# Performance work log

Measured on AMD Instinct MI355X. Metric: run time of the kernel, lower is better.

## Reference

```python
import jax, jax.numpy as jnp
import numpy as np

D_MODEL = 1024
NUM_HEADS = 16
DEPTH = D_MODEL // NUM_HEADS


def setup_inputs() -> dict:
    key = jax.random.key(0)
    ks = jax.random.split(key, 6)
    B, S = 2, 2048
    scale = 1.0 / np.sqrt(D_MODEL)
    return {
        "q": jax.random.normal(ks[0], (B, S, D_MODEL), jnp.float32),
        "k": jax.random.normal(ks[1], (B, S, D_MODEL), jnp.float32),
        "v": jax.random.normal(ks[2], (B, S, D_MODEL), jnp.float32),
        "wq": jax.random.normal(ks[3], (D_MODEL, D_MODEL), jnp.float32) * scale,
        "wk": jax.random.normal(ks[4], (D_MODEL, D_MODEL), jnp.float32) * scale,
        "wv": jax.random.normal(ks[5], (D_MODEL, D_MODEL), jnp.float32) * scale,
    }


def reference(q, k, v, wq, wk, wv):
    B, S, _ = q.shape
    # Linear projections (nn.Linear: x @ W.T), then split heads -> [B,H,S,depth]
    def split(x):
        return x.reshape(B, -1, NUM_HEADS, DEPTH).transpose(0, 2, 1, 3)
    Q = split(q @ wq.T)
    K = split(k @ wk.T)
    V = split(v @ wv.T)
    scores = jnp.einsum("bhqd,bhkd->bhqk", Q, K) / np.sqrt(DEPTH).astype(np.float32)
    attn = jax.nn.softmax(scores, axis=-1)
    out = jnp.einsum("bhqk,bhkd->bhqd", attn, V)
    # merge heads; note: original forward never applies self.dense
    return out.transpose(0, 2, 1, 3).reshape(B, S, D_MODEL)
```

## Files before the change

kernel.cpp:

```cpp
#include <hip/hip_runtime.h>
#include <hip/hip_bf16.h>
#include <stdint.h>

#define B_SZ 2
#define S_LEN 2048
#define DM 1024
#define NH 16
#define DEPTH 64
#define M_ROWS (B_SZ * S_LEN)
#define SCALE_Q 0.1803368801111144f

typedef __attribute__((ext_vector_type(8))) short bf16x8;
typedef __attribute__((ext_vector_type(4))) float f32x4;

__device__ __forceinline__ unsigned short f2bf(float x) {
    union { float f; unsigned u; } a; a.f = x;
    unsigned r = a.u + 0x7FFF + ((a.u >> 16) & 1);
    return (unsigned short)(r >> 16);
}

__device__ __forceinline__ void async_ld16(const unsigned short* g, unsigned short* l) {
    __builtin_amdgcn_global_load_lds(
        (const __attribute__((address_space(1))) void*)g,
        (__attribute__((address_space(3))) void*)l,
        16, 0, 0);
}


__global__ __launch_bounds__(256)
void convert_kernel(const float* __restrict__ q, const float* __restrict__ k,
                    const float* __restrict__ v, const float* __restrict__ wq,
                    const float* __restrict__ wk, const float* __restrict__ wv,
                    unsigned short* __restrict__ dst) {
    const int z = blockIdx.y;
    const float* src = (z == 0) ? q : (z == 1) ? k : (z == 2) ? v
                     : (z == 3) ? wq : (z == 4) ? wk : wv;
    const size_t n4  = (z < 3) ? ((size_t)M_ROWS * DM / 4) : ((size_t)DM * DM / 4);
    const size_t off = (z < 3) ? ((size_t)z * M_ROWS * DM)
                               : ((size_t)3 * M_ROWS * DM + (size_t)(z - 3) * DM * DM);
    unsigned short* d = dst + off;
    const size_t stride = (size_t)gridDim.x * blockDim.x;
    for (size_t i = (size_t)blockIdx.x * blockDim.x + threadIdx.x; i < n4; i += stride) {
        float4 x = ((const float4*)src)[i];
        ushort4 p;
        p.x = f2bf(x.x); p.y = f2bf(x.y); p.z = f2bf(x.z); p.w = f2bf(x.w);
        ((ushort4*)d)[i] = p;
    }
}

__global__ __launch_bounds__(256)
void proj_gemm2_kernel(const unsigned short* __restrict__ Xall,
                       const unsigned short* __restrict__ Wall,
                       unsigned short* __restrict__ Call) {
    __shared__ unsigned short As[128 * 64];
    __shared__ unsigned short Bs[128 * 64];

    const int z = blockIdx.z;
    const unsigned short* X = Xall + (size_t)z * M_ROWS * DM;
    const unsigned short* W = Wall + (size_t)z * DM * DM;
    unsigned short* C = Call + (size_t)z * M_ROWS * DM;

    const int tid  = threadIdx.x;
    const int wave = tid >> 6;
    const int lane = tid & 63;
    const int quad = lane >> 4;
    const int l16  = lane & 15;
    const int m0 = blockIdx.x * 128;
    const int n0 = blockIdx.y * 128;
    const int wm = (wave >> 1) * 64;
    const int wn = (wave & 1) * 64;

    const int sr = lane >> 3;
    const int sc = (lane & 7) ^ sr;

    f32x4 acc[4][4];
#pragma unroll
    for (int mt = 0; mt < 4; ++mt)
#pragma unroll
        for (int nt = 0; nt < 4; ++nt)
            acc[mt][nt] = (f32x4){0.f, 0.f, 0.f, 0.f};

    for (int k0 = 0; k0 < DM; k0 += 64) {
#pragma unroll
        for (int i = 0; i < 4; ++i) {
            const int r = i * 32 + wave * 8 + sr;
            async_ld16(X + (size_t)(m0 + r) * DM + k0 + sc * 8,
                       (unsigned short*)((char*)As + i * 4096 + wave * 1024));
            async_ld16(W + (size_t)(n0 + r) * DM + k0 + sc * 8,
                       (unsigned short*)((char*)Bs + i * 4096 + wave * 1024));
        }
        __syncthreads();

#pragma unroll
        for (int kc = 0; kc < 2; ++kc) {
            bf16x8 af[4], bfr[4];
#pragma unroll
            for (int mt = 0; mt < 4; ++mt) {
                const int row = wm + mt * 16 + l16;
                af[mt] = *(const bf16x8*)&As[row * 64 + (((kc * 4 + quad) ^ (row & 7)) * 8)];
            }
#pragma unroll
            for (int nt = 0; nt < 4; ++nt) {
                const int row = wn + nt * 16 + l16;
                bfr[nt] = *(const bf16x8*)&Bs[row * 64 + (((kc * 4 + quad) ^ (row & 7)) * 8)];
            }
#pragma unroll
            for (int mt = 0; mt < 4; ++mt)
#pragma unroll
                for (int nt = 0; nt < 4; ++nt)
                    acc[mt][nt] = __builtin_amdgcn_mfma_f32_16x16x32_bf16(
                        af[mt], bfr[nt], acc[mt][nt], 0, 0, 0);
        }
        __syncthreads();
    }

    const float scale = (z == 0) ? SCALE_Q : 1.0f;
#pragma unroll
    for (int mt = 0; mt < 4; ++mt)
#pragma unroll
        for (int nt = 0; nt < 4; ++nt)
#pragma unroll
            for (int r = 0; r < 4; ++r) {
                const int row = m0 + wm + mt * 16 + quad * 4 + r;
                const int col = n0 + wn + nt * 16 + l16;
                C[(size_t)row * DM + col] = f2bf(acc[mt][nt][r] * scale);
            }
}

__global__ __launch_bounds__(256)
void vtrans_kernel(const unsigned short* __restrict__ Vp,
                   unsigned short* __restrict__ Vt) {
    __shared__ unsigned short Ls[64 * 72];
    const int tr = blockIdx.x;
    const int h  = blockIdx.y;
    const int tid = threadIdx.x;

#pragma unroll
    for (int i = 0; i < 2; ++i) {
        const int id = i * 256 + tid;
        const int r = id >> 3, c = id & 7;
        bf16x8 v8 = *(const bf16x8*)&Vp[(size_t)(tr * 64 + r) * DM + h * 64 + c * 8];
        *(bf16x8*)&Ls[r * 72 + ((c ^ (r & 7)) * 8)] = v8;
    }
    __syncthreads();

    const int b = tr >> 5;
    const int col0 = (tr & 31) * 64;
#pragma unroll
    for (int i = 0; i < 2; ++i) {
        const int id = i * 256 + tid;
        const int d = id >> 3, c2 = id & 7;
        unsigned short tmp[8];
#pragma unroll
        for (int j = 0; j < 8; ++j) {
            const int t = c2 * 8 + j;
            tmp[j] = Ls[t * 72 + (((d >> 3) ^ (t & 7)) * 8) + (d & 7)];
        }
        *(bf16x8*)&Vt[(size_t)((b * NH + h) * DEPTH + d) * S_LEN + col0 + c2 * 8] =
            *(const bf16x8*)tmp;
    }
}

__global__ __launch_bounds__(256)
void attn2_kernel(const unsigned short* __restrict__ Qp,
                  const unsigned short* __restrict__ Kp,
                  const unsigned short* __restrict__ Vt,
                  float* __restrict__ out) {
    __shared__ unsigned short Ks[64 * 64];
    __shared__ unsigned short Vs[64 * 64];
    __shared__ unsigned short Ps[4 * 16 * 72];

    const int tid  = threadIdx.x;
    const int wave = tid >> 6;
    const int lane = tid & 63;
    const int quad = lane >> 4;
    const int l16  = lane & 15;
    const int q0 = blockIdx.x * 64;
    const int h  = blockIdx.y;
    const int b  = blockIdx.z;

    const int sr = lane >> 3;
    const int sc = (lane & 7) ^ sr;

    const unsigned short* Kg = Kp + (size_t)(b * S_LEN) * DM + h * DEPTH;
    const unsigned short* Vg = Vt + (size_t)((b * NH + h) * DEPTH) * S_LEN;

    bf16x8 qf[2];
    {
        const unsigned short* p =
            Qp + (size_t)(b * S_LEN + q0 + wave * 16 + l16) * DM + h * DEPTH;
        qf[0] = *(const bf16x8*)(p + quad * 8);
        qf[1] = *(const bf16x8*)(p + 32 + quad * 8);
    }

    f32x4 accO[4];
    float lacc[4];
#pragma unroll
    for (int f = 0; f < 4; ++f) accO[f] = (f32x4){0.f, 0.f, 0.f, 0.f};
#pragma unroll
    for (int r = 0; r < 4; ++r) lacc[r] = 0.f;

    unsigned short* PsW = &Ps[wave * 16 * 72];

    for (int t0 = 0; t0 < S_LEN; t0 += 64) {
#pragma unroll
        for (int i = 0; i < 2; ++i) {
            const int r = i * 32 + wave * 8 + sr;
            async_ld16(Kg + (size_t)(t0 + r) * DM + sc * 8,
                       (unsigned short*)((char*)Ks + i * 4096 + wave * 1024));
            async_ld16(Vg + (size_t)r * S_LEN + t0 + sc * 8,
                       (unsigned short*)((char*)Vs + i * 4096 + wave * 1024));
        }
        __syncthreads();

        f32x4 sc4[4];
#pragma unroll
        for (int nt = 0; nt < 4; ++nt) {
            const int row = nt * 16 + l16;
            bf16x8 kf0 = *(const bf16x8*)&Ks[row * 64 + ((quad ^ (row & 7)) * 8)];
            bf16x8 kf1 = *(const bf16x8*)&Ks[row * 64 + (((4 + quad) ^ (row & 7)) * 8)];
            f32x4 a = (f32x4){0.f, 0.f, 0.f, 0.f};
            a = __builtin_amdgcn_mfma_f32_16x16x32_bf16(qf[0], kf0, a, 0, 0, 0);
            a = __builtin_amdgcn_mfma_f32_16x16x32_bf16(qf[1], kf1, a, 0, 0, 0);
            sc4[nt] = a;
        }

#pragma unroll
        for (int nt = 0; nt < 4; ++nt)
#pragma unroll
            for (int r = 0; r < 4; ++r) {
                float p = __builtin_amdgcn_exp2f(sc4[nt][r]);
                union { float f; unsigned u; } cv; cv.f = p;
                union { unsigned u; float f; } tv; tv.u = cv.u & 0xFFFF0000u;
                lacc[r] += tv.f;
                PsW[(quad * 4 + r) * 72 + nt * 16 + l16] = (unsigned short)(cv.u >> 16);
            }

        bf16x8 pf0 = *(const bf16x8*)&PsW[l16 * 72 + quad * 8];
        bf16x8 pf1 = *(const bf16x8*)&PsW[l16 * 72 + 32 + quad * 8];

#pragma unroll
        for (int f = 0; f < 4; ++f) {
            const int row = f * 16 + l16;
            bf16x8 vf0 = *(const bf16x8*)&Vs[row * 64 + ((quad ^ (row & 7)) * 8)];
            bf16x8 vf1 = *(const bf16x8*)&Vs[row * 64 + (((4 + quad) ^ (row & 7)) * 8)];
            accO[f] = __builtin_amdgcn_mfma_f32_16x16x32_bf16(pf0, vf0, accO[f], 0, 0, 0);
            accO[f] = __builtin_amdgcn_mfma_f32_16x16x32_bf16(pf1, vf1, accO[f], 0, 0, 0);
        }
        __syncthreads();
    }

#pragma unroll
    for (int r = 0; r < 4; ++r)
#pragma unroll
        for (int off = 1; off < 16; off <<= 1)
            lacc[r] += __shfl_xor(lacc[r], off, 64);

#pragma unroll
    for (int f = 0; f < 4; ++f)
#pragma unroll
        for (int r = 0; r < 4; ++r) {
            const size_t row = (size_t)(b * S_LEN + q0 + wave * 16 + quad * 4 + r);
            out[row * DM + h * DEPTH + f * 16 + l16] = accO[f][r] / lacc[r];
        }
}

#define LDK 72

__global__ __launch_bounds__(256)
void proj_gemm_kernel(const float* __restrict__ q, const float* __restrict__ k,
                      const float* __restrict__ v, const float* __restrict__ wq,
                      const float* __restrict__ wk, const float* __restrict__ wv,
                      unsigned short* __restrict__ Qp, unsigned short* __restrict__ Kp,
                      unsigned short* __restrict__ Vp) {
    __shared__ unsigned short As[128 * LDK];
    __shared__ unsigned short Bs[128 * LDK];

    const int z = blockIdx.z;
    const float* __restrict__ X = (z == 0) ? q : (z == 1) ? k : v;
    const float* __restrict__ W = (z == 0) ? wq : (z == 1) ? wk : wv;
    unsigned short* __restrict__ C = (z == 0) ? Qp : (z == 1) ? Kp : Vp;

    const int tid  = threadIdx.x;
    const int wave = tid >> 6;
    const int lane = tid & 63;
    const int quad = lane >> 4;
    const int l16  = lane & 15;
    const int m0 = blockIdx.x * 128;
    const int n0 = blockIdx.y * 128;
    const int wm = (wave >> 1) * 64;
    const int wn = (wave & 1) * 64;

    f32x4 acc[4][4];
#pragma unroll
    for (int mt = 0; mt < 4; ++mt)
#pragma unroll
        for (int nt = 0; nt < 4; ++nt)
            acc[mt][nt] = (f32x4){0.f, 0.f, 0.f, 0.f};

    for (int k0 = 0; k0 < DM; k0 += 64) {
#pragma unroll
        for (int vv = 0; vv < 8; ++vv) {
            int vecid = tid + 256 * vv;
            int r  = vecid >> 4;
            int c4 = vecid & 15;
            const float4 xa = *(const float4*)&X[(size_t)(m0 + r) * DM + k0 + c4 * 4];
            ushort4 pa;
            pa.x = f2bf(xa.x); pa.y = f2bf(xa.y); pa.z = f2bf(xa.z); pa.w = f2bf(xa.w);
            *(ushort4*)&As[r * LDK + c4 * 4] = pa;
            const float4 xb = *(const float4*)&W[(size_t)(n0 + r) * DM + k0 + c4 * 4];
            ushort4 pb;
            pb.x = f2bf(xb.x); pb.y = f2bf(xb.y); pb.z = f2bf(xb.z); pb.w = f2bf(xb.w);
            *(ushort4*)&Bs[r * LDK + c4 * 4] = pb;
        }
        __syncthreads();

#pragma unroll
        for (int kc = 0; kc < 2; ++kc) {
            bf16x8 af[4], bfr[4];
#pragma unroll
            for (int mt = 0; mt < 4; ++mt)
                af[mt] = *(const bf16x8*)&As[(wm + mt * 16 + l16) * LDK + kc * 32 + quad * 8];
#pragma unroll
            for (int nt = 0; nt < 4; ++nt)
                bfr[nt] = *(const bf16x8*)&Bs[(wn + nt * 16 + l16) * LDK + kc * 32 + quad * 8];
#pragma unroll
            for (int mt = 0; mt < 4; ++mt)
#pragma unroll
                for (int nt = 0; nt < 4; ++nt)
                    acc[mt][nt] = __builtin_amdgcn_mfma_f32_16x16x32_bf16(
                        af[mt], bfr[nt], acc[mt][nt], 0, 0, 0);
        }
        __syncthreads();
    }

#pragma unroll
    for (int mt = 0; mt < 4; ++mt)
#pragma unroll
        for (int nt = 0; nt < 4; ++nt)
#pragma unroll
            for (int r = 0; r < 4; ++r) {
                int row = m0 + wm + mt * 16 + quad * 4 + r;
                int col = n0 + wn + nt * 16 + l16;
                C[(size_t)row * DM + col] = f2bf(acc[mt][nt][r]);
            }
}

__global__ __launch_bounds__(256)
void attn_kernel(const unsigned short* __restrict__ Qp,
                 const unsigned short* __restrict__ Kp,
                 const unsigned short* __restrict__ Vp,
                 float* __restrict__ out) {
    __shared__ unsigned short Ks[64 * LDK];
    __shared__ unsigned short Vtl[64 * LDK];
    __shared__ unsigned short Ps[4 * 16 * LDK];

    const int tid  = threadIdx.x;
    const int wave = tid >> 6;
    const int lane = tid & 63;
    const int quad = lane >> 4;
    const int l16  = lane & 15;
    const int q0 = blockIdx.x * 64;
    const int h  = blockIdx.y;
    const int b  = blockIdx.z;
    const int wbase = wave * 16 * LDK;

    bf16x8 qf[2];
    {
        size_t row = (size_t)b * S_LEN + q0 + wave * 16 + l16;
        const unsigned short* p = Qp + row * DM + h * DEPTH;
        qf[0] = *(const bf16x8*)(p + quad * 8);
        qf[1] = *(const bf16x8*)(p + 32 + quad * 8);
    }

    float m_i[4], l_i[4];
    f32x4 accO[4];
#pragma unroll
    for (int r = 0; r < 4; ++r) { m_i[r] = -1e30f; l_i[r] = 0.f; }
#pragma unroll
    for (int f = 0; f < 4; ++f) accO[f] = (f32x4){0.f, 0.f, 0.f, 0.f};

    for (int t0 = 0; t0 < S_LEN; t0 += 64) {
#pragma unroll
        for (int vv = 0; vv < 2; ++vv) {
            int vecid = tid + 256 * vv;
            int r  = vecid >> 3;
            int cv = vecid & 7;
            size_t grow = (size_t)(b * S_LEN + t0 + r) * DM + h * DEPTH + cv * 8;
            *(bf16x8*)&Ks[r * LDK + cv * 8] = *(const bf16x8*)(Kp + grow);
            bf16x8 vvv = *(const bf16x8*)(Vp + grow);
#pragma unroll
            for (int j = 0; j < 8; ++j)
                Vtl[(cv * 8 + j) * LDK + r] = ((const unsigned short*)&vvv)[j];
        }
        __syncthreads();

        f32x4 sc4[4];
#pragma unroll
        for (int nt = 0; nt < 4; ++nt) {
            f32x4 a = (f32x4){0.f, 0.f, 0.f, 0.f};
            bf16x8 kf0 = *(const bf16x8*)&Ks[(nt * 16 + l16) * LDK + quad * 8];
            bf16x8 kf1 = *(const bf16x8*)&Ks[(nt * 16 + l16) * LDK + 32 + quad * 8];
            a = __builtin_amdgcn_mfma_f32_16x16x32_bf16(qf[0], kf0, a, 0, 0, 0);
            a = __builtin_amdgcn_mfma_f32_16x16x32_bf16(qf[1], kf1, a, 0, 0, 0);
            sc4[nt] = a;
        }
#pragma unroll
        for (int nt = 0; nt < 4; ++nt)
#pragma unroll
            for (int r = 0; r < 4; ++r) sc4[nt][r] *= 0.125f;

#pragma unroll
        for (int r = 0; r < 4; ++r) {
            float mx = fmaxf(fmaxf(sc4[0][r], sc4[1][r]), fmaxf(sc4[2][r], sc4[3][r]));
#pragma unroll
            for (int off = 1; off < 16; off <<= 1)
                mx = fmaxf(mx, __shfl_xor(mx, off, 64));
            float mnew = fmaxf(m_i[r], mx);
            float alpha = __expf(m_i[r] - mnew);
            float rs = 0.f;
#pragma unroll
            for (int nt = 0; nt < 4; ++nt) {
                float p = __expf(sc4[nt][r] - mnew);
                sc4[nt][r] = p;
                rs += p;
            }
#pragma unroll
            for (int off = 1; off < 16; off <<= 1)
                rs += __shfl_xor(rs, off, 64);
            l_i[r] = l_i[r] * alpha + rs;
            m_i[r] = mnew;
#pragma unroll
            for (int f = 0; f < 4; ++f) accO[f][r] *= alpha;
        }

#pragma unroll
        for (int nt = 0; nt < 4; ++nt)
#pragma unroll
            for (int r = 0; r < 4; ++r)
                Ps[wbase + (quad * 4 + r) * LDK + nt * 16 + l16] = f2bf(sc4[nt][r]);
        __syncthreads();

        bf16x8 pf0 = *(const bf16x8*)&Ps[wbase + l16 * LDK + quad * 8];
        bf16x8 pf1 = *(const bf16x8*)&Ps[wbase + l16 * LDK + 32 + quad * 8];
#pragma unroll
        for (int f = 0; f < 4; ++f) {
            bf16x8 vf0 = *(const bf16x8*)&Vtl[(f * 16 + l16) * LDK + quad * 8];
            bf16x8 vf1 = *(const bf16x8*)&Vtl[(f * 16 + l16) * LDK + 32 + quad * 8];
            accO[f] = __builtin_amdgcn_mfma_f32_16x16x32_bf16(pf0, vf0, accO[f], 0, 0, 0);
            accO[f] = __builtin_amdgcn_mfma_f32_16x16x32_bf16(pf1, vf1, accO[f], 0, 0, 0);
        }
        __syncthreads();
    }

#pragma unroll
    for (int f = 0; f < 4; ++f)
#pragma unroll
        for (int r = 0; r < 4; ++r) {
            size_t row = (size_t)b * S_LEN + q0 + wave * 16 + quad * 4 + r;
            out[row * DM + h * DEPTH + f * 16 + l16] = accO[f][r] / l_i[r];
        }
}

extern "C" void kernel_launch(void* const* d_in, const int* in_sizes, int n_in,
                              void* d_out, int out_size, void* d_ws, size_t ws_size,
                              hipStream_t stream) {
    const float* q  = (const float*)d_in[0];
    const float* k  = (const float*)d_in[1];
    const float* v  = (const float*)d_in[2];
    const float* wq = (const float*)d_in[3];
    const float* wk = (const float*)d_in[4];
    const float* wv = (const float*)d_in[5];
    float* out = (float*)d_out;

    unsigned short* ws = (unsigned short*)d_ws;
    const size_t NPROJ = (size_t)M_ROWS * DM;
    const size_t NW    = (size_t)DM * DM;

    const size_t need = (3 * NPROJ + 3 * NW + 3 * NPROJ) * sizeof(unsigned short);

    if (ws_size >= need) {
        unsigned short* Xbf = ws;
        unsigned short* Wbf = ws + 3 * NPROJ;
        unsigned short* Cp  = ws + 3 * NPROJ + 3 * NW;
        unsigned short* Qp  = Cp;
        unsigned short* Kp  = Cp + NPROJ;
        unsigned short* Vp  = Cp + 2 * NPROJ;
        unsigned short* Vt  = ws;

        convert_kernel<<<dim3(256, 6), 256, 0, stream>>>(q, k, v, wq, wk, wv, Xbf);
        proj_gemm2_kernel<<<dim3(M_ROWS / 128, DM / 128, 3), 256, 0, stream>>>(Xbf, Wbf, Cp);
        vtrans_kernel<<<dim3(M_ROWS / 64, NH), 256, 0, stream>>>(Vp, Vt);
        attn2_kernel<<<dim3(S_LEN / 64, NH, B_SZ), 256, 0, stream>>>(Qp, Kp, Vt, out);
    } else {
        unsigned short* Qp = ws;
        unsigned short* Kp = ws + NPROJ;
        unsigned short* Vp = ws + 2 * NPROJ;
        proj_gemm_kernel<<<dim3(M_ROWS / 128, DM / 128, 3), 256, 0, stream>>>(
            q, k, v, wq, wk, wv, Qp, Kp, Vp);
        attn_kernel<<<dim3(S_LEN / 64, NH, B_SZ), 256, 0, stream>>>(Qp, Kp, Vp, out);
    }
}
```

Before: 214.2 us.

## Switch projection GEMM and attention to 32x32x16 MFMA with larger query tiles

Both the projection GEMM and the attention kernel move from 16x16x32 to 32x32x16 bf16 MFMA tiles. Attention blocks now cover 128 queries (32 per wave), which halves K/V reloads per query. The V transpose permutes key order so the packed P stores line up with the new layout. The aim is fewer fragment LDS reads per flop and higher MFMA throughput, at the cost of more accumulator registers and possibly lower occupancy, with only half as many attention blocks.

```diff
diff --git a/kernel.cpp b/kernel.cpp
--- a/kernel.cpp
+++ b/kernel.cpp
@@ -12,6 +12,7 @@
 
 typedef __attribute__((ext_vector_type(8))) short bf16x8;
 typedef __attribute__((ext_vector_type(4))) float f32x4;
+typedef __attribute__((ext_vector_type(16))) float f32x16;
 
 __device__ __forceinline__ unsigned short f2bf(float x) {
     union { float f; unsigned u; } a; a.f = x;
@@ -19,7 +20,7 @@
     return (unsigned short)(r >> 16);
 }
 
-__device__ __forceinline__ void async_ld16(const unsigned short* g, unsigned short* l) {
+__device__ __forceinline__ void async_ld16(const unsigned short* g, void* l) {
     __builtin_amdgcn_global_load_lds(
         (const __attribute__((address_space(1))) void*)g,
         (__attribute__((address_space(3))) void*)l,
@@ -49,7 +50,7 @@
 }
 
 __global__ __launch_bounds__(256)
-void proj_gemm2_kernel(const unsigned short* __restrict__ Xall,
+void proj_gemm3_kernel(const unsigned short* __restrict__ Xall,
                        const unsigned short* __restrict__ Wall,
                        unsigned short* __restrict__ Call) {
     __shared__ unsigned short As[128 * 64];
@@ -63,67 +64,68 @@
     const int tid  = threadIdx.x;
     const int wave = tid >> 6;
     const int lane = tid & 63;
-    const int quad = lane >> 4;
-    const int l16  = lane & 15;
+    const int l32  = lane & 31;
+    const int s    = lane >> 5;
     const int m0 = blockIdx.x * 128;
     const int n0 = blockIdx.y * 128;
     const int wm = (wave >> 1) * 64;
     const int wn = (wave & 1) * 64;
 
-    const int sr = lane >> 3;
-    const int sc = (lane & 7) ^ sr;
-
-    f32x4 acc[4][4];
-#pragma unroll
-    for (int mt = 0; mt < 4; ++mt)
-#pragma unroll
-        for (int nt = 0; nt < 4; ++nt)
-            acc[mt][nt] = (f32x4){0.f, 0.f, 0.f, 0.f};
+    const int r8 = lane >> 3;
+    const int sc = (lane & 7) ^ r8;
+
+    f32x16 acc[2][2];
+#pragma unroll
+    for (int mi = 0; mi < 2; ++mi)
+#pragma unroll
+        for (int ni = 0; ni < 2; ++ni)
+#pragma unroll
+            for (int r = 0; r < 16; ++r) acc[mi][ni][r] = 0.f;
 
     for (int k0 = 0; k0 < DM; k0 += 64) {
 #pragma unroll
         for (int i = 0; i < 4; ++i) {
-            const int r = i * 32 + wave * 8 + sr;
+            const int r = i * 32 + wave * 8 + r8;
             async_ld16(X + (size_t)(m0 + r) * DM + k0 + sc * 8,
-                       (unsigned short*)((char*)As + i * 4096 + wave * 1024));
+                       (char*)As + i * 4096 + wave * 1024);
             async_ld16(W + (size_t)(n0 + r) * DM + k0 + sc * 8,
-                       (unsigned short*)((char*)Bs + i * 4096 + wave * 1024));
-        }
-        __syncthreads();
-
-#pragma unroll
-        for (int kc = 0; kc < 2; ++kc) {
-            bf16x8 af[4], bfr[4];
-#pragma unroll
-            for (int mt = 0; mt < 4; ++mt) {
-                const int row = wm + mt * 16 + l16;
-                af[mt] = *(const bf16x8*)&As[row * 64 + (((kc * 4 + quad) ^ (row & 7)) * 8)];
-            }
-#pragma unroll
-            for (int nt = 0; nt < 4; ++nt) {
-                const int row = wn + nt * 16 + l16;
-                bfr[nt] = *(const bf16x8*)&Bs[row * 64 + (((kc * 4 + quad) ^ (row & 7)) * 8)];
-            }
-#pragma unroll
-            for (int mt = 0; mt < 4; ++mt)
-#pragma unroll
-                for (int nt = 0; nt < 4; ++nt)
-                    acc[mt][nt] = __builtin_amdgcn_mfma_f32_16x16x32_bf16(
-                        af[mt], bfr[nt], acc[mt][nt], 0, 0, 0);
+                       (char*)Bs + i * 4096 + wave * 1024);
+        }
+        __syncthreads();
+
+#pragma unroll
+        for (int ch = 0; ch < 4; ++ch) {
+            bf16x8 af[2], bfr[2];
+#pragma unroll
+            for (int mi = 0; mi < 2; ++mi) {
+                const int row = wm + mi * 32 + l32;
+                af[mi] = *(const bf16x8*)&As[row * 64 + (((2 * ch + s) ^ (row & 7)) * 8)];
+            }
+#pragma unroll
+            for (int ni = 0; ni < 2; ++ni) {
+                const int row = wn + ni * 32 + l32;
+                bfr[ni] = *(const bf16x8*)&Bs[row * 64 + (((2 * ch + s) ^ (row & 7)) * 8)];
+            }
+#pragma unroll
+            for (int mi = 0; mi < 2; ++mi)
+#pragma unroll
+                for (int ni = 0; ni < 2; ++ni)
+                    acc[mi][ni] = __builtin_amdgcn_mfma_f32_32x32x16_bf16(
+                        af[mi], bfr[ni], acc[mi][ni], 0, 0, 0);
         }
         __syncthreads();
     }
 
     const float scale = (z == 0) ? SCALE_Q : 1.0f;
 #pragma unroll
-    for (int mt = 0; mt < 4; ++mt)
-#pragma unroll
-        for (int nt = 0; nt < 4; ++nt)
-#pragma unroll
-            for (int r = 0; r < 4; ++r) {
-                const int row = m0 + wm + mt * 16 + quad * 4 + r;
-                const int col = n0 + wn + nt * 16 + l16;
-                C[(size_t)row * DM + col] = f2bf(acc[mt][nt][r] * scale);
+    for (int mi = 0; mi < 2; ++mi)
+#pragma unroll
+        for (int ni = 0; ni < 2; ++ni)
+#pragma unroll
+            for (int r = 0; r < 16; ++r) {
+                const int row = m0 + wm + mi * 32 + (r & 3) + 8 * (r >> 2) + 4 * s;
+                const int col = n0 + wn + ni * 32 + l32;
+                C[(size_t)row * DM + col] = f2bf(acc[mi][ni][r] * scale);
             }
 }
 
@@ -153,7 +155,8 @@
         unsigned short tmp[8];
 #pragma unroll
         for (int j = 0; j < 8; ++j) {
-            const int t = c2 * 8 + j;
+            const int cc = c2 * 8 + j;
+            const int t = (cc >> 1) + ((cc & 1) << 5);
             tmp[j] = Ls[t * 72 + (((d >> 3) ^ (t & 7)) * 8) + (d & 7)];
         }
         *(bf16x8*)&Vt[(size_t)((b * NH + h) * DEPTH + d) * S_LEN + col0 + c2 * 8] =
@@ -162,106 +165,121 @@
 }
 
 __global__ __launch_bounds__(256)
-void attn2_kernel(const unsigned short* __restrict__ Qp,
+void attn3_kernel(const unsigned short* __restrict__ Qp,
                   const unsigned short* __restrict__ Kp,
                   const unsigned short* __restrict__ Vt,
                   float* __restrict__ out) {
     __shared__ unsigned short Ks[64 * 64];
     __shared__ unsigned short Vs[64 * 64];
-    __shared__ unsigned short Ps[4 * 16 * 72];
+    __shared__ unsigned short Ps[4 * 32 * 72];
 
     const int tid  = threadIdx.x;
     const int wave = tid >> 6;
     const int lane = tid & 63;
-    const int quad = lane >> 4;
-    const int l16  = lane & 15;
-    const int q0 = blockIdx.x * 64;
+    const int l32  = lane & 31;
+    const int s    = lane >> 5;
+    const int q0 = blockIdx.x * 128;
     const int h  = blockIdx.y;
     const int b  = blockIdx.z;
 
-    const int sr = lane >> 3;
-    const int sc = (lane & 7) ^ sr;
+    const int r8 = lane >> 3;
+    const int sc = (lane & 7) ^ r8;
 
     const unsigned short* Kg = Kp + (size_t)(b * S_LEN) * DM + h * DEPTH;
     const unsigned short* Vg = Vt + (size_t)((b * NH + h) * DEPTH) * S_LEN;
 
-    bf16x8 qf[2];
+    bf16x8 qf[4];
     {
         const unsigned short* p =
-            Qp + (size_t)(b * S_LEN + q0 + wave * 16 + l16) * DM + h * DEPTH;
-        qf[0] = *(const bf16x8*)(p + quad * 8);
-        qf[1] = *(const bf16x8*)(p + 32 + quad * 8);
-    }
-
-    f32x4 accO[4];
-    float lacc[4];
-#pragma unroll
-    for (int f = 0; f < 4; ++f) accO[f] = (f32x4){0.f, 0.f, 0.f, 0.f};
-#pragma unroll
-    for (int r = 0; r < 4; ++r) lacc[r] = 0.f;
-
-    unsigned short* PsW = &Ps[wave * 16 * 72];
+            Qp + (size_t)(b * S_LEN + q0 + wave * 32 + l32) * DM + h * DEPTH;
+#pragma unroll
+        for (int ch = 0; ch < 4; ++ch)
+            qf[ch] = *(const bf16x8*)(p + ch * 16 + s * 8);
+    }
+
+    f32x16 oacc[2];
+    float lacc[16];
+#pragma unroll
+    for (int d = 0; d < 2; ++d)
+#pragma unroll
+        for (int r = 0; r < 16; ++r) oacc[d][r] = 0.f;
+#pragma unroll
+    for (int r = 0; r < 16; ++r) lacc[r] = 0.f;
+
+    unsigned short* PsW = &Ps[wave * 32 * 72];
 
     for (int t0 = 0; t0 < S_LEN; t0 += 64) {
 #pragma unroll
         for (int i = 0; i < 2; ++i) {
-            const int r = i * 32 + wave * 8 + sr;
+            const int r = i * 32 + wave * 8 + r8;
             async_ld16(Kg + (size_t)(t0 + r) * DM + sc * 8,
-                       (unsigned short*)((char*)Ks + i * 4096 + wave * 1024));
+                       (char*)Ks + i * 4096 + wave * 1024);
             async_ld16(Vg + (size_t)r * S_LEN + t0 + sc * 8,
-                       (unsigned short*)((char*)Vs + i * 4096 + wave * 1024));
-        }
-        __syncthreads();
-
-        f32x4 sc4[4];
-#pragma unroll
-        for (int nt = 0; nt < 4; ++nt) {
-            const int row = nt * 16 + l16;
-            bf16x8 kf0 = *(const bf16x8*)&Ks[row * 64 + ((quad ^ (row & 7)) * 8)];
-            bf16x8 kf1 = *(const bf16x8*)&Ks[row * 64 + (((4 + quad) ^ (row & 7)) * 8)];
-            f32x4 a = (f32x4){0.f, 0.f, 0.f, 0.f};
-            a = __builtin_amdgcn_mfma_f32_16x16x32_bf16(qf[0], kf0, a, 0, 0, 0);
-            a = __builtin_amdgcn_mfma_f32_16x16x32_bf16(qf[1], kf1, a, 0, 0, 0);
-            sc4[nt] = a;
-        }
-
-#pragma unroll
-        for (int nt = 0; nt < 4; ++nt)
-#pragma unroll
-            for (int r = 0; r < 4; ++r) {
-                float p = __builtin_amdgcn_exp2f(sc4[nt][r]);
-                union { float f; unsigned u; } cv; cv.f = p;
-                union { unsigned u; float f; } tv; tv.u = cv.u & 0xFFFF0000u;
-                lacc[r] += tv.f;
-                PsW[(quad * 4 + r) * 72 + nt * 16 + l16] = (unsigned short)(cv.u >> 16);
-            }
-
-        bf16x8 pf0 = *(const bf16x8*)&PsW[l16 * 72 + quad * 8];
-        bf16x8 pf1 = *(const bf16x8*)&PsW[l16 * 72 + 32 + quad * 8];
-
-#pragma unroll
-        for (int f = 0; f < 4; ++f) {
-            const int row = f * 16 + l16;
-            bf16x8 vf0 = *(const bf16x8*)&Vs[row * 64 + ((quad ^ (row & 7)) * 8)];
-            bf16x8 vf1 = *(const bf16x8*)&Vs[row * 64 + (((4 + quad) ^ (row & 7)) * 8)];
-            accO[f] = __builtin_amdgcn_mfma_f32_16x16x32_bf16(pf0, vf0, accO[f], 0, 0, 0);
-            accO[f] = __builtin_amdgcn_mfma_f32_16x16x32_bf16(pf1, vf1, accO[f], 0, 0, 0);
-        }
-        __syncthreads();
-    }
-
-#pragma unroll
-    for (int r = 0; r < 4; ++r)
-#pragma unroll
-        for (int off = 1; off < 16; off <<= 1)
+                       (char*)Vs + i * 4096 + wave * 1024);
+        }
+        __syncthreads();
+
+        f32x16 sacc[2];
+#pragma unroll
+        for (int tb = 0; tb < 2; ++tb) {
+#pragma unroll
+            for (int r = 0; r < 16; ++r) sacc[tb][r] = 0.f;
+            const int trow = tb * 32 + l32;
+#pragma unroll
+            for (int ch = 0; ch < 4; ++ch) {
+                bf16x8 kf = *(const bf16x8*)
+                    &Ks[trow * 64 + (((2 * ch + s) ^ (trow & 7)) * 8)];
+                sacc[tb] = __builtin_amdgcn_mfma_f32_32x32x16_bf16(
+                    qf[ch], kf, sacc[tb], 0, 0, 0);
+            }
+        }
+
+#pragma unroll
+        for (int r = 0; r < 16; ++r) {
+            const float p0 = __builtin_amdgcn_exp2f(sacc[0][r]);
+            const float p1 = __builtin_amdgcn_exp2f(sacc[1][r]);
+            union { float f; unsigned u; } a0, a1;
+            a0.f = p0; a1.f = p1;
+            union { unsigned u; float f; } t0f, t1f;
+            t0f.u = a0.u & 0xFFFF0000u;
+            t1f.u = a1.u & 0xFFFF0000u;
+            lacc[r] += t0f.f + t1f.f;
+            const unsigned pk = (a0.u >> 16) | (a1.u & 0xFFFF0000u);
+            const int qrow = (r & 3) + 8 * (r >> 2) + 4 * s;
+            *(unsigned*)&PsW[qrow * 72 + 2 * l32] = pk;
+        }
+
+        bf16x8 pf[4];
+#pragma unroll
+        for (int ch = 0; ch < 4; ++ch)
+            pf[ch] = *(const bf16x8*)&PsW[l32 * 72 + ch * 16 + s * 8];
+#pragma unroll
+        for (int db = 0; db < 2; ++db) {
+            const int drow = db * 32 + l32;
+#pragma unroll
+            for (int ch = 0; ch < 4; ++ch) {
+                bf16x8 vf = *(const bf16x8*)
+                    &Vs[drow * 64 + (((2 * ch + s) ^ (drow & 7)) * 8)];
+                oacc[db] = __builtin_amdgcn_mfma_f32_32x32x16_bf16(
+                    pf[ch], vf, oacc[db], 0, 0, 0);
+            }
+        }
+        __syncthreads();
+    }
+
+#pragma unroll
+    for (int r = 0; r < 16; ++r)
+#pragma unroll
+        for (int off = 1; off < 32; off <<= 1)
             lacc[r] += __shfl_xor(lacc[r], off, 64);
 
 #pragma unroll
-    for (int f = 0; f < 4; ++f)
-#pragma unroll
-        for (int r = 0; r < 4; ++r) {
-            const size_t row = (size_t)(b * S_LEN + q0 + wave * 16 + quad * 4 + r);
-            out[row * DM + h * DEPTH + f * 16 + l16] = accO[f][r] / lacc[r];
+    for (int db = 0; db < 2; ++db)
+#pragma unroll
+        for (int r = 0; r < 16; ++r) {
+            const int qrow = (r & 3) + 8 * (r >> 2) + 4 * s;
+            const size_t row = (size_t)(b * S_LEN + q0 + wave * 32 + qrow);
+            out[row * DM + h * DEPTH + db * 32 + l32] = oacc[db][r] / lacc[r];
         }
 }
 
@@ -489,9 +507,9 @@
         unsigned short* Vt  = ws;
 
         convert_kernel<<<dim3(256, 6), 256, 0, stream>>>(q, k, v, wq, wk, wv, Xbf);
-        proj_gemm2_kernel<<<dim3(M_ROWS / 128, DM / 128, 3), 256, 0, stream>>>(Xbf, Wbf, Cp);
+        proj_gemm3_kernel<<<dim3(M_ROWS / 128, DM / 128, 3), 256, 0, stream>>>(Xbf, Wbf, Cp);
         vtrans_kernel<<<dim3(M_ROWS / 64, NH), 256, 0, stream>>>(Vp, Vt);
-        attn2_kernel<<<dim3(S_LEN / 64, NH, B_SZ), 256, 0, stream>>>(Qp, Kp, Vt, out);
+        attn3_kernel<<<dim3(S_LEN / 128, NH, B_SZ), 256, 0, stream>>>(Qp, Kp, Vt, out);
     } else {
         unsigned short* Qp = ws;
         unsigned short* Kp = ws + NPROJ;
```

New measurement: 203.1 us. 5.2% less time.
